# Performance work log

Hardware: AMD Instinct MI355X
Metric: run time of the kernel (lower is better)

Reference implementation:

```python
import jax, jax.numpy as jnp
import numpy as np

# dims: B scenes, V views, T tokens per view, D=d1=d2 embed dim, H=4*D mlp hidden
B, V, T, D = 2, 8, 512, 1024
H = 4 * D
LN_EPS = 1e-5


def setup_inputs() -> dict:
    key = jax.random.key(0)
    ks = jax.random.split(key, 9)
    x = jax.random.normal(ks[0], (B, V, T, D), jnp.float32)
    theta_Q = jax.random.normal(ks[1], (D, D), jnp.float32)  # Task.theta_Q ~ randn
    # TTT_MLP params (nn.Linear default-init scale approximated; exact dist irrelevant for math)
    W1 = jax.random.normal(ks[2], (D, H), jnp.float32) * (1.0 / np.sqrt(D))
    b1 = jnp.zeros((H,), jnp.float32)
    W2 = jax.random.normal(ks[3], (H, D), jnp.float32) * (1.0 / np.sqrt(H))
    b2 = jnp.zeros((D,), jnp.float32)
    gamma = jnp.ones((D,), jnp.float32)   # LayerNorm weight
    beta = jnp.zeros((D,), jnp.float32)   # LayerNorm bias
    alpha = jnp.full((1, D), 0.01, jnp.float32)
    return {"x": x, "theta_Q": theta_Q, "W1": W1, "b1": b1, "W2": W2,
            "b2": b2, "gamma": gamma, "beta": beta, "alpha": alpha}


def _layernorm(y, gamma, beta):
    mu = jnp.mean(y, axis=-1, keepdims=True)
    var = jnp.mean(jnp.square(y - mu), axis=-1, keepdims=True)  # biased, as torch LayerNorm
    return (y - mu) * jax.lax.rsqrt(var + LN_EPS) * gamma + beta


def reference(x, theta_Q, W1, b1, W2, b2, gamma, beta, alpha):
    # NOTE: in the original module, update_model rebinds a local (`p = p - lr*g`),
    # so the learner params are NEVER updated; proxy_loss/grads are dead code w.r.t.
    # the output. Faithful math: out = TTT_MLP(x @ theta_Q), fully parallel over tokens.
    z = jnp.einsum('bvtd,de->bvte', x, theta_Q)          # [B,V,T,D]
    h = jax.nn.gelu(z @ W1 + b1, approximate=False)      # exact erf GELU, as torch nn.GELU
    y = h @ W2 + b2                                      # [B,V,T,D]
    ln = _layernorm(y, gamma, beta)
    return z + jnp.tanh(alpha) * ln
```

## Files before the change

### kernel.cpp

```cpp
#include <hip/hip_runtime.h>
#include <hip/hip_bf16.h>
#include <cstdint>
#include <math.h>

typedef __hip_bfloat16 bf16_t;
typedef __attribute__((ext_vector_type(8))) __bf16 bf16x8;
typedef __attribute__((ext_vector_type(4))) float f32x4;

static_assert(sizeof(bf16x8) == 16, "bf16x8 must be 4 VGPRs");

static constexpr int DD = 1024;
static constexpr int HH = 4096;

#define GLD16(gp, lp)                                                                              \
  __builtin_amdgcn_global_load_lds(                                                                \
      (__attribute__((address_space(1))) void*)(uintptr_t)(gp),                                    \
      (__attribute__((address_space(3))) void*)(uint32_t)(uintptr_t)(lp), 16, 0, 0)

#if !__has_builtin(__builtin_amdgcn_exp2f)
#define __builtin_amdgcn_exp2f(x) exp2f(x)
#endif
#if !__has_builtin(__builtin_amdgcn_rcpf)
#define __builtin_amdgcn_rcpf(x) (1.0f / (x))
#endif

__device__ __forceinline__ float fast_gelu(float u) {
  const float t = __builtin_amdgcn_exp2f(-2.4554089f * u);
  return u * __builtin_amdgcn_rcpf(1.0f + t);
}

__global__ __launch_bounds__(256) void k_split_x(const float* __restrict__ x,
                                                 bf16_t* __restrict__ xh,
                                                 bf16_t* __restrict__ xl, int n4) {
  int i = blockIdx.x * 256 + threadIdx.x;
  const int stride = gridDim.x * 256;
  for (; i < n4; i += stride) {
    const float4 v = reinterpret_cast<const float4*>(x)[i];
    float vv[4] = {v.x, v.y, v.z, v.w};
    union { bf16_t b[4]; short4 s; } H, L;
#pragma unroll
    for (int j = 0; j < 4; ++j) {
      H.b[j] = __float2bfloat16(vv[j]);
      L.b[j] = __float2bfloat16(vv[j] - __bfloat162float(H.b[j]));
    }
    reinterpret_cast<short4*>(xh)[i] = H.s;
    reinterpret_cast<short4*>(xl)[i] = L.s;
  }
}

template <bool SPLIT>
__global__ __launch_bounds__(256) void k_transpose(const float* __restrict__ W,
                                                   bf16_t* __restrict__ Th,
                                                   bf16_t* __restrict__ Tl, int K, int N) {
  __shared__ float tile[32][33];
  const int n0 = blockIdx.x * 32, k0 = blockIdx.y * 32;
  const int tx = threadIdx.x, ty = threadIdx.y;
#pragma unroll
  for (int r = 0; r < 4; ++r) {
    const int k = ty + r * 8;
    tile[k][tx] = W[(size_t)(k0 + k) * N + n0 + tx];
  }
  __syncthreads();
#pragma unroll
  for (int r = 0; r < 4; ++r) {
    const int n = ty + r * 8;
    const float v = tile[tx][n];
    const bf16_t h = __float2bfloat16(v);
    Th[(size_t)(n0 + n) * K + k0 + tx] = h;
    if (SPLIT) Tl[(size_t)(n0 + n) * K + k0 + tx] = __float2bfloat16(v - __bfloat162float(h));
  }
}

__global__ __launch_bounds__(256) void k_gemm_split(const bf16_t* __restrict__ Ah,
                                                    const bf16_t* __restrict__ Al,
                                                    const bf16_t* __restrict__ BTh,
                                                    const bf16_t* __restrict__ BTl,
                                                    float* __restrict__ Cf,
                                                    bf16_t* __restrict__ Cb,
                                                    int M, int N, int K) {
  constexpr int BM = 128, BN = 128, BK = 32;
  __shared__ __align__(16) bf16_t sAh[BM * BK];
  __shared__ __align__(16) bf16_t sBh[BN * BK];
  __shared__ __align__(16) bf16_t sAl[BM * BK];
  __shared__ __align__(16) bf16_t sBl[BN * BK];

  const int nbn = N / BN;
  const int nwg = gridDim.x;
  const int wg = blockIdx.x;
  const int cpx = nwg >> 3;
  const int swz = (wg & 7) * cpx + (wg >> 3);
  const int bm = swz / nbn, bn = swz % nbn;

  const int t = threadIdx.x;
  const int l = t & 63;
  const int w = t >> 6;
  const int wr = (w >> 1) * 64, wc = (w & 1) * 64;

  const size_t Abase = (size_t)bm * BM * K;
  const size_t Bbase = (size_t)bn * BN * K;

  const int r0 = t >> 2, kc0 = (t & 3) * 8;
  const int r1 = r0 + 64;

  f32x4 acc[4][4] = {};
  const int lm = l & 15;
  const int l4 = l >> 4;
  const int kb8 = l4 * 8;

  const int nk = K / BK;
  for (int kt = 0; kt < nk; ++kt) {
    const size_t gk = (size_t)kt * BK;
    GLD16(Ah + Abase + (size_t)r0 * K + gk + kc0, &sAh[r0 * BK + kc0]);
    GLD16(Ah + Abase + (size_t)r1 * K + gk + kc0, &sAh[r1 * BK + kc0]);
    GLD16(BTh + Bbase + (size_t)r0 * K + gk + kc0, &sBh[r0 * BK + kc0]);
    GLD16(BTh + Bbase + (size_t)r1 * K + gk + kc0, &sBh[r1 * BK + kc0]);
    GLD16(Al + Abase + (size_t)r0 * K + gk + kc0, &sAl[r0 * BK + kc0]);
    GLD16(Al + Abase + (size_t)r1 * K + gk + kc0, &sAl[r1 * BK + kc0]);
    GLD16(BTl + Bbase + (size_t)r0 * K + gk + kc0, &sBl[r0 * BK + kc0]);
    GLD16(BTl + Bbase + (size_t)r1 * K + gk + kc0, &sBl[r1 * BK + kc0]);
    __syncthreads();

    bf16x8 a[4], b[4];
#pragma unroll
    for (int m = 0; m < 4; ++m)
      a[m] = *reinterpret_cast<const bf16x8*>(&sAh[(wr + m * 16 + lm) * BK + kb8]);
#pragma unroll
    for (int n = 0; n < 4; ++n)
      b[n] = *reinterpret_cast<const bf16x8*>(&sBh[(wc + n * 16 + lm) * BK + kb8]);
#pragma unroll
    for (int m = 0; m < 4; ++m)
#pragma unroll
      for (int n = 0; n < 4; ++n)
        acc[m][n] = __builtin_amdgcn_mfma_f32_16x16x32_bf16(a[m], b[n], acc[m][n], 0, 0, 0);

    {
      bf16x8 al_[4], bl_[4];
#pragma unroll
      for (int m = 0; m < 4; ++m)
        al_[m] = *reinterpret_cast<const bf16x8*>(&sAl[(wr + m * 16 + lm) * BK + kb8]);
#pragma unroll
      for (int n = 0; n < 4; ++n)
        bl_[n] = *reinterpret_cast<const bf16x8*>(&sBl[(wc + n * 16 + lm) * BK + kb8]);
#pragma unroll
      for (int m = 0; m < 4; ++m)
#pragma unroll
        for (int n = 0; n < 4; ++n) {
          acc[m][n] = __builtin_amdgcn_mfma_f32_16x16x32_bf16(a[m], bl_[n], acc[m][n], 0, 0, 0);
          acc[m][n] = __builtin_amdgcn_mfma_f32_16x16x32_bf16(al_[m], b[n], acc[m][n], 0, 0, 0);
        }
    }
    __syncthreads();
  }

  const int cr = l4 * 4;
#pragma unroll
  for (int m = 0; m < 4; ++m) {
#pragma unroll
    for (int n = 0; n < 4; ++n) {
      const int c = bn * BN + wc + n * 16 + lm;
#pragma unroll
      for (int j = 0; j < 4; ++j) {
        const int r = bm * BM + wr + m * 16 + cr + j;
        const size_t idx = (size_t)r * N + c;
        const float v = acc[m][n][j];
        Cf[idx] = v;
        Cb[idx] = __float2bfloat16(v);
      }
    }
  }
}

template <int EPI>
__global__ __launch_bounds__(512, 2) void k_gemm_256(const bf16_t* __restrict__ A,
                                                     const bf16_t* __restrict__ BT,
                                                     const float* __restrict__ bias,
                                                     float* __restrict__ Cf,
                                                     bf16_t* __restrict__ Cb,
                                                     int M, int N, int K, int LDK) {
  constexpr int BM = 256, BN = 256, BK = 32;
  __shared__ __align__(16) bf16_t sA[2][BM * BK];
  __shared__ __align__(16) bf16_t sB[2][BN * BK];

  const int nbn = N / BN;
  const int nwg = gridDim.x;
  const int wg = blockIdx.x;
  const int cpx = nwg >> 3;
  const int swz = (wg & 7) * cpx + (wg >> 3);
  const int bm = swz / nbn, bn = swz % nbn;

  const int ks = blockIdx.y;
  const size_t k0 = (size_t)ks * K;
  Cf += (size_t)ks * M * N;

  const int t = threadIdx.x;
  const int l = t & 63;
  const int w = t >> 6;
  const int wr = (w >> 2) * 128;
  const int wc = (w & 3) * 64;

  const size_t Abase = (size_t)bm * BM * LDK + k0;
  const size_t Bbase = (size_t)bn * BN * LDK + k0;

  const int lm = l & 15;
  const int l4 = l >> 4;

  auto stage = [&](int kt, int pb) {
    const size_t gk = (size_t)kt * BK;
#pragma unroll
    for (int p = 0; p < 2; ++p) {
      const int c = t + 512 * p;
      const int r = c >> 2, j = c & 3;
      const int jg = (j ^ (r & 3)) * 8;
      GLD16(A + Abase + (size_t)r * LDK + gk + jg, &sA[pb][c * 8]);
    }
#pragma unroll
    for (int p = 0; p < 2; ++p) {
      const int c = t + 512 * p;
      const int r = c >> 2, j = c & 3;
      const int jg = (j ^ (r & 3)) * 8;
      GLD16(BT + Bbase + (size_t)r * LDK + gk + jg, &sB[pb][c * 8]);
    }
  };

  f32x4 acc[8][4] = {};
  const int nk = K / BK;

  stage(0, 0);
  stage(1, 1);
  for (int kt = 0; kt < nk; ++kt) {
    const int pb = kt & 1;
    if (kt + 1 < nk) {
      asm volatile("s_waitcnt vmcnt(4)" ::: "memory");
    } else {
      asm volatile("s_waitcnt vmcnt(0)" ::: "memory");
    }
    __builtin_amdgcn_s_barrier();
    __builtin_amdgcn_sched_barrier(0);

    bf16x8 b[4];
#pragma unroll
    for (int n = 0; n < 4; ++n) {
      const int R = wc + n * 16 + lm;
      const int q = l4 ^ (R & 3);
      b[n] = *reinterpret_cast<const bf16x8*>(&sB[pb][R * BK + q * 8]);
    }
    {
      bf16x8 a[4];
#pragma unroll
      for (int m = 0; m < 4; ++m) {
        const int R = wr + m * 16 + lm;
        const int q = l4 ^ (R & 3);
        a[m] = *reinterpret_cast<const bf16x8*>(&sA[pb][R * BK + q * 8]);
      }
      asm volatile("s_waitcnt lgkmcnt(0)" ::: "memory");
      __builtin_amdgcn_sched_barrier(0);
      __builtin_amdgcn_s_setprio(1);
#pragma unroll
      for (int m = 0; m < 4; ++m)
#pragma unroll
        for (int n = 0; n < 4; ++n)
          acc[m][n] = __builtin_amdgcn_mfma_f32_16x16x32_bf16(a[m], b[n], acc[m][n], 0, 0, 0);
      __builtin_amdgcn_s_setprio(0);
    }
    __builtin_amdgcn_s_barrier();
    {
      bf16x8 a[4];
#pragma unroll
      for (int m = 0; m < 4; ++m) {
        const int R = wr + 64 + m * 16 + lm;
        const int q = l4 ^ (R & 3);
        a[m] = *reinterpret_cast<const bf16x8*>(&sA[pb][R * BK + q * 8]);
      }
      asm volatile("s_waitcnt lgkmcnt(0)" ::: "memory");
      __builtin_amdgcn_sched_barrier(0);
      __builtin_amdgcn_s_setprio(1);
#pragma unroll
      for (int m = 0; m < 4; ++m)
#pragma unroll
        for (int n = 0; n < 4; ++n)
          acc[4 + m][n] = __builtin_amdgcn_mfma_f32_16x16x32_bf16(a[m], b[n], acc[4 + m][n], 0, 0, 0);
      __builtin_amdgcn_s_setprio(0);
    }
    __builtin_amdgcn_sched_barrier(0);
    __builtin_amdgcn_s_barrier();
    if (kt + 2 < nk) stage(kt + 2, pb);
  }

  const int cr = l4 * 4;
#pragma unroll
  for (int m = 0; m < 8; ++m) {
    const int rbase = bm * BM + wr + ((m < 4) ? m * 16 : 64 + (m - 4) * 16);
#pragma unroll
    for (int n = 0; n < 4; ++n) {
      const int c = bn * BN + wc + n * 16 + lm;
      const float bc = (EPI == 2) ? bias[c] : 0.0f;
#pragma unroll
      for (int j = 0; j < 4; ++j) {
        const int r = rbase + cr + j;
        const size_t idx = (size_t)r * N + c;
        const float v = acc[m][n][j];
        if (EPI == 2) {
          Cb[idx] = __float2bfloat16(fast_gelu(v + bc));
        } else {
          Cf[idx] = v;
        }
      }
    }
  }
}

__global__ __launch_bounds__(256) void k_ln_res(const float* __restrict__ y0,
                                                const float* __restrict__ y1,
                                                const float* __restrict__ b2,
                                                const float* __restrict__ z,
                                                const float* __restrict__ gamma,
                                                const float* __restrict__ beta,
                                                const float* __restrict__ alpha,
                                                float* __restrict__ out) {
  const int row = blockIdx.x;
  const int t = threadIdx.x;
  const float4 va = reinterpret_cast<const float4*>(y0 + (size_t)row * DD)[t];
  const float4 vb = reinterpret_cast<const float4*>(y1 + (size_t)row * DD)[t];
  const float4 bc = reinterpret_cast<const float4*>(b2)[t];
  float4 v;
  v.x = va.x + vb.x + bc.x; v.y = va.y + vb.y + bc.y;
  v.z = va.z + vb.z + bc.z; v.w = va.w + vb.w + bc.w;
  float s = v.x + v.y + v.z + v.w;
  float q = v.x * v.x + v.y * v.y + v.z * v.z + v.w * v.w;
#pragma unroll
  for (int m = 1; m < 64; m <<= 1) {
    s += __shfl_xor(s, m, 64);
    q += __shfl_xor(q, m, 64);
  }
  __shared__ float ss[4], sq[4];
  if ((t & 63) == 0) { ss[t >> 6] = s; sq[t >> 6] = q; }
  __syncthreads();
  s = ss[0] + ss[1] + ss[2] + ss[3];
  q = sq[0] + sq[1] + sq[2] + sq[3];
  const float mu = s * (1.0f / DD);
  const float var = fmaxf(q * (1.0f / DD) - mu * mu, 0.0f);
  const float rs = rsqrtf(var + 1e-5f);
  const float4 g = reinterpret_cast<const float4*>(gamma)[t];
  const float4 bb = reinterpret_cast<const float4*>(beta)[t];
  const float4 aa = reinterpret_cast<const float4*>(alpha)[t];
  const float4 zz = reinterpret_cast<const float4*>(z + (size_t)row * DD)[t];
  float4 o;
  o.x = zz.x + tanhf(aa.x) * ((v.x - mu) * rs * g.x + bb.x);
  o.y = zz.y + tanhf(aa.y) * ((v.y - mu) * rs * g.y + bb.y);
  o.z = zz.z + tanhf(aa.z) * ((v.z - mu) * rs * g.z + bb.z);
  o.w = zz.w + tanhf(aa.w) * ((v.w - mu) * rs * g.w + bb.w);
  reinterpret_cast<float4*>(out + (size_t)row * DD)[t] = o;
}

extern "C" void kernel_launch(void* const* d_in, const int* in_sizes, int n_in, void* d_out,
                              int out_size, void* d_ws, size_t ws_size, hipStream_t stream) {
  const float* x   = (const float*)d_in[0];
  const float* thQ = (const float*)d_in[1];
  const float* W1  = (const float*)d_in[2];
  const float* b1  = (const float*)d_in[3];
  const float* W2  = (const float*)d_in[4];
  const float* b2  = (const float*)d_in[5];
  const float* gam = (const float*)d_in[6];
  const float* bet = (const float*)d_in[7];
  const float* alp = (const float*)d_in[8];
  float* out = (float*)d_out;

  const int M = in_sizes[0] / DD;

  char* ws = (char*)d_ws;
  size_t off = 0;
  auto take = [&](size_t bytes) -> char* {
    char* p = ws + off;
    off += (bytes + 255) & ~(size_t)255;
    return p;
  };
  bf16_t* xh  = (bf16_t*)take((size_t)M * DD * 2);
  bf16_t* xl  = (bf16_t*)take((size_t)M * DD * 2);
  bf16_t* qTh = (bf16_t*)take((size_t)DD * DD * 2);
  bf16_t* qTl = (bf16_t*)take((size_t)DD * DD * 2);
  bf16_t* w1T = (bf16_t*)take((size_t)DD * HH * 2);
  bf16_t* w2T = (bf16_t*)take((size_t)HH * DD * 2);
  float*  zf  = (float*)take((size_t)M * DD * 4);
  bf16_t* zb  = (bf16_t*)take((size_t)M * DD * 2);
  bf16_t* hb  = (bf16_t*)take((size_t)M * HH * 2);
  float*  yf  = (float*)take((size_t)M * DD * 4 * 2);

  hipLaunchKernelGGL(k_split_x, dim3(2048), dim3(256), 0, stream, x, xh, xl, M * DD / 4);
  hipLaunchKernelGGL((k_transpose<true>), dim3(DD / 32, DD / 32), dim3(32, 8), 0, stream,
                     thQ, qTh, qTl, DD, DD);
  hipLaunchKernelGGL((k_transpose<false>), dim3(HH / 32, DD / 32), dim3(32, 8), 0, stream,
                     W1, w1T, (bf16_t*)nullptr, DD, HH);
  hipLaunchKernelGGL((k_transpose<false>), dim3(DD / 32, HH / 32), dim3(32, 8), 0, stream,
                     W2, w2T, (bf16_t*)nullptr, HH, DD);

  hipLaunchKernelGGL(k_gemm_split, dim3((M / 128) * (DD / 128)), dim3(256), 0, stream,
                     xh, xl, qTh, qTl, zf, zb, M, DD, DD);
  hipLaunchKernelGGL((k_gemm_256<2>), dim3((M / 256) * (HH / 256)), dim3(512), 0, stream,
                     zb, w1T, b1, (float*)nullptr, hb, M, HH, DD, DD);
  hipLaunchKernelGGL((k_gemm_256<3>), dim3((M / 256) * (DD / 256), 2), dim3(512), 0, stream,
                     hb, w2T, (const float*)nullptr, yf, (bf16_t*)nullptr, M, DD, HH / 2, HH);
  hipLaunchKernelGGL(k_ln_res, dim3(M), dim3(256), 0, stream,
                     yf, yf + (size_t)M * DD, b2, zf, gam, bet, alp, out);
}
```

Baseline: 360.8 us.

## Double-buffer split-precision GEMM, change LDS swizzle, relax main GEMM waits

The split bf16 hi/lo GEMM (used for x@theta_Q) now double-buffers its LDS tiles and prefetches two k-steps ahead, waiting with vmcnt instead of a full syncthreads before each step. This is meant to overlap global loads with MFMA work. The main GEMM's XOR swizzle now keys on (row>>2)&3 instead of row&3 to reduce LDS bank conflicts. Its mid-iteration barrier and explicit lgkmcnt waits are removed and one setprio region spans both MFMA halves, giving the compiler more freedom to interleave. The double buffer doubles the split kernel's LDS use to 64KB, which may cut occupancy.

```diff
diff --git a/kernel.cpp b/kernel.cpp
--- a/kernel.cpp
+++ b/kernel.cpp
@@ -79,10 +79,10 @@
                                                     bf16_t* __restrict__ Cb,
                                                     int M, int N, int K) {
   constexpr int BM = 128, BN = 128, BK = 32;
-  __shared__ __align__(16) bf16_t sAh[BM * BK];
-  __shared__ __align__(16) bf16_t sBh[BN * BK];
-  __shared__ __align__(16) bf16_t sAl[BM * BK];
-  __shared__ __align__(16) bf16_t sBl[BN * BK];
+  __shared__ __align__(16) bf16_t sAh[2][BM * BK];
+  __shared__ __align__(16) bf16_t sBh[2][BN * BK];
+  __shared__ __align__(16) bf16_t sAl[2][BM * BK];
+  __shared__ __align__(16) bf16_t sBl[2][BN * BK];
 
   const int nbn = N / BN;
   const int nwg = gridDim.x;
@@ -107,26 +107,38 @@
   const int l4 = l >> 4;
   const int kb8 = l4 * 8;
 
+  auto stage = [&](int kt, int pb) {
+    const size_t gk = (size_t)kt * BK;
+    GLD16(Ah + Abase + (size_t)r0 * K + gk + kc0, &sAh[pb][r0 * BK + kc0]);
+    GLD16(Ah + Abase + (size_t)r1 * K + gk + kc0, &sAh[pb][r1 * BK + kc0]);
+    GLD16(BTh + Bbase + (size_t)r0 * K + gk + kc0, &sBh[pb][r0 * BK + kc0]);
+    GLD16(BTh + Bbase + (size_t)r1 * K + gk + kc0, &sBh[pb][r1 * BK + kc0]);
+    GLD16(Al + Abase + (size_t)r0 * K + gk + kc0, &sAl[pb][r0 * BK + kc0]);
+    GLD16(Al + Abase + (size_t)r1 * K + gk + kc0, &sAl[pb][r1 * BK + kc0]);
+    GLD16(BTl + Bbase + (size_t)r0 * K + gk + kc0, &sBl[pb][r0 * BK + kc0]);
+    GLD16(BTl + Bbase + (size_t)r1 * K + gk + kc0, &sBl[pb][r1 * BK + kc0]);
+  };
+
   const int nk = K / BK;
+  stage(0, 0);
+  stage(1, 1);
   for (int kt = 0; kt < nk; ++kt) {
-    const size_t gk = (size_t)kt * BK;
-    GLD16(Ah + Abase + (size_t)r0 * K + gk + kc0, &sAh[r0 * BK + kc0]);
-    GLD16(Ah + Abase + (size_t)r1 * K + gk + kc0, &sAh[r1 * BK + kc0]);
-    GLD16(BTh + Bbase + (size_t)r0 * K + gk + kc0, &sBh[r0 * BK + kc0]);
-    GLD16(BTh + Bbase + (size_t)r1 * K + gk + kc0, &sBh[r1 * BK + kc0]);
-    GLD16(Al + Abase + (size_t)r0 * K + gk + kc0, &sAl[r0 * BK + kc0]);
-    GLD16(Al + Abase + (size_t)r1 * K + gk + kc0, &sAl[r1 * BK + kc0]);
-    GLD16(BTl + Bbase + (size_t)r0 * K + gk + kc0, &sBl[r0 * BK + kc0]);
-    GLD16(BTl + Bbase + (size_t)r1 * K + gk + kc0, &sBl[r1 * BK + kc0]);
-    __syncthreads();
+    const int pb = kt & 1;
+    if (kt + 1 < nk) {
+      asm volatile("s_waitcnt vmcnt(8)" ::: "memory");
+    } else {
+      asm volatile("s_waitcnt vmcnt(0)" ::: "memory");
+    }
+    __builtin_amdgcn_s_barrier();
+    __builtin_amdgcn_sched_barrier(0);
 
     bf16x8 a[4], b[4];
 #pragma unroll
     for (int m = 0; m < 4; ++m)
-      a[m] = *reinterpret_cast<const bf16x8*>(&sAh[(wr + m * 16 + lm) * BK + kb8]);
+      a[m] = *reinterpret_cast<const bf16x8*>(&sAh[pb][(wr + m * 16 + lm) * BK + kb8]);
 #pragma unroll
     for (int n = 0; n < 4; ++n)
-      b[n] = *reinterpret_cast<const bf16x8*>(&sBh[(wc + n * 16 + lm) * BK + kb8]);
+      b[n] = *reinterpret_cast<const bf16x8*>(&sBh[pb][(wc + n * 16 + lm) * BK + kb8]);
 #pragma unroll
     for (int m = 0; m < 4; ++m)
 #pragma unroll
@@ -137,10 +149,10 @@
       bf16x8 al_[4], bl_[4];
 #pragma unroll
       for (int m = 0; m < 4; ++m)
-        al_[m] = *reinterpret_cast<const bf16x8*>(&sAl[(wr + m * 16 + lm) * BK + kb8]);
+        al_[m] = *reinterpret_cast<const bf16x8*>(&sAl[pb][(wr + m * 16 + lm) * BK + kb8]);
 #pragma unroll
       for (int n = 0; n < 4; ++n)
-        bl_[n] = *reinterpret_cast<const bf16x8*>(&sBl[(wc + n * 16 + lm) * BK + kb8]);
+        bl_[n] = *reinterpret_cast<const bf16x8*>(&sBl[pb][(wc + n * 16 + lm) * BK + kb8]);
 #pragma unroll
       for (int m = 0; m < 4; ++m)
 #pragma unroll
@@ -149,7 +161,10 @@
           acc[m][n] = __builtin_amdgcn_mfma_f32_16x16x32_bf16(al_[m], b[n], acc[m][n], 0, 0, 0);
         }
     }
-    __syncthreads();
+
+    __builtin_amdgcn_sched_barrier(0);
+    __builtin_amdgcn_s_barrier();
+    if (kt + 2 < nk) stage(kt + 2, pb);
   }
 
   const int cr = l4 * 4;
@@ -210,14 +225,14 @@
     for (int p = 0; p < 2; ++p) {
       const int c = t + 512 * p;
       const int r = c >> 2, j = c & 3;
-      const int jg = (j ^ (r & 3)) * 8;
+      const int jg = (j ^ ((r >> 2) & 3)) * 8;
       GLD16(A + Abase + (size_t)r * LDK + gk + jg, &sA[pb][c * 8]);
     }
 #pragma unroll
     for (int p = 0; p < 2; ++p) {
       const int c = t + 512 * p;
       const int r = c >> 2, j = c & 3;
-      const int jg = (j ^ (r & 3)) * 8;
+      const int jg = (j ^ ((r >> 2) & 3)) * 8;
       GLD16(BT + Bbase + (size_t)r * LDK + gk + jg, &sB[pb][c * 8]);
     }
   };
@@ -241,46 +256,40 @@
 #pragma unroll
     for (int n = 0; n < 4; ++n) {
       const int R = wc + n * 16 + lm;
-      const int q = l4 ^ (R & 3);
+      const int q = l4 ^ ((R >> 2) & 3);
       b[n] = *reinterpret_cast<const bf16x8*>(&sB[pb][R * BK + q * 8]);
     }
+    __builtin_amdgcn_s_setprio(1);
     {
       bf16x8 a[4];
 #pragma unroll
       for (int m = 0; m < 4; ++m) {
         const int R = wr + m * 16 + lm;
-        const int q = l4 ^ (R & 3);
+        const int q = l4 ^ ((R >> 2) & 3);
         a[m] = *reinterpret_cast<const bf16x8*>(&sA[pb][R * BK + q * 8]);
       }
-      asm volatile("s_waitcnt lgkmcnt(0)" ::: "memory");
-      __builtin_amdgcn_sched_barrier(0);
-      __builtin_amdgcn_s_setprio(1);
 #pragma unroll
       for (int m = 0; m < 4; ++m)
 #pragma unroll
         for (int n = 0; n < 4; ++n)
           acc[m][n] = __builtin_amdgcn_mfma_f32_16x16x32_bf16(a[m], b[n], acc[m][n], 0, 0, 0);
-      __builtin_amdgcn_s_setprio(0);
-    }
-    __builtin_amdgcn_s_barrier();
+    }
     {
       bf16x8 a[4];
 #pragma unroll
       for (int m = 0; m < 4; ++m) {
         const int R = wr + 64 + m * 16 + lm;
-        const int q = l4 ^ (R & 3);
+        const int q = l4 ^ ((R >> 2) & 3);
         a[m] = *reinterpret_cast<const bf16x8*>(&sA[pb][R * BK + q * 8]);
       }
-      asm volatile("s_waitcnt lgkmcnt(0)" ::: "memory");
-      __builtin_amdgcn_sched_barrier(0);
-      __builtin_amdgcn_s_setprio(1);
 #pragma unroll
       for (int m = 0; m < 4; ++m)
 #pragma unroll
         for (int n = 0; n < 4; ++n)
           acc[4 + m][n] = __builtin_amdgcn_mfma_f32_16x16x32_bf16(a[m], b[n], acc[4 + m][n], 0, 0, 0);
-      __builtin_amdgcn_s_setprio(0);
-    }
+    }
+    __builtin_amdgcn_s_setprio(0);
+
     __builtin_amdgcn_sched_barrier(0);
     __builtin_amdgcn_s_barrier();
     if (kt + 2 < nk) stage(kt + 2, pb);
```

New measurement: 353.6 us. 2.0% less time.
